# Kernel tuning notes

Measured on AMD Instinct MI355X. Metric: run time of the kernel, lower is better.

Reference implementation:

```python
import jax, jax.numpy as jnp
import numpy as np

N = 50000   # n_nodes (cells)
E = 800000  # n_edges (avg degree 16)
D = 128     # feature dim


def setup_inputs() -> dict:
    key = jax.random.key(0)
    ks = jax.random.split(key, 8)
    x = jax.random.normal(ks[0], (N, D), dtype=jnp.float32)
    src = jax.random.randint(ks[1], (E,), 0, N, dtype=jnp.int32)
    dst = jax.random.randint(ks[2], (E,), 0, N, dtype=jnp.int32)
    vals = jax.random.uniform(ks[3], (E,), dtype=jnp.float32)
    # GraphConvolution weight (dim -> dim), applied as x @ W
    W_gc = jax.random.normal(ks[4], (D, D), dtype=jnp.float32) / np.sqrt(D).astype(np.float32)
    b_gc = jnp.zeros((D,), jnp.float32)
    # linear2: nn.Linear(dim, dim) -> x @ W2.T + b2
    W2 = jax.random.normal(ks[5], (D, D), dtype=jnp.float32) / np.sqrt(D).astype(np.float32)
    b2 = jnp.zeros((D,), jnp.float32)
    return {"x": x, "vals": vals, "W_gc": W_gc, "b_gc": b_gc,
            "W2": W2, "b2": b2, "src": src, "dst": dst}


def reference(x, vals, W_gc, b_gc, W2, b2, src, dst):
    # GraphConvolution (dropout is identity in eval mode):
    #   support = x @ W + b ; out = relu(adj_sparse @ support)
    support = x @ W_gc + b_gc                         # [N, D]
    msg = support[src] * vals[:, None]                # gather rows, scale by edge weight
    agg = jax.ops.segment_sum(msg, dst, num_segments=N)  # SpMM via scatter-add
    x1 = jax.nn.relu(agg)                             # [N, D]
    # linear2 + dropout(eval=identity) + detached L2 row-normalize
    x2 = x1 @ W2.T + b2                               # [N, D]
    nrm = jax.lax.stop_gradient(
        jnp.sqrt(jnp.sum(x2 * x2, axis=1, keepdims=True)))
    return x2 / nrm
```

## Files before the change

kernel.cpp:

```cpp
#include <hip/hip_runtime.h>
#include <hip/hip_bf16.h>

#define N_NODES 50000
#define N_EDGES 800000
#define DIM     128
#define N_STRIPS (N_NODES / 16)
#define N_BKT    196
#define EDGE_CHUNKS 196
#define BCAP     8192
#define EBUF_CAP 7168
#define AGS      68
#define GEMM_BLOCKS ((N_STRIPS + 3) / 4)
#define FRONT_BLOCKS (GEMM_BLOCKS + EDGE_CHUNKS)

typedef short short8 __attribute__((ext_vector_type(8)));
typedef float floatx4 __attribute__((ext_vector_type(4)));

__device__ inline unsigned short f2bf(float f) {
    __hip_bfloat16 h = __float2bfloat16(f);
    return *reinterpret_cast<unsigned short*>(&h);
}

__global__ __launch_bounds__(256) void pre_pack(
    const float* __restrict__ W1, const float* __restrict__ W2,
    uint4* __restrict__ p1, uint4* __restrict__ p2, int* __restrict__ bcnt)
{
    const int blk = blockIdx.x;
    const int t   = threadIdx.x;
    if (blk < 8) {
        const int s    = blk * 256 + t;
        const int lane = s & 63;
        const int nt   = (s >> 6) & 7;
        const int ks   = s >> 9;
        const int m    = lane & 15;
        const int q    = lane >> 4;
        unsigned short e[8];
        #pragma unroll
        for (int j = 0; j < 8; ++j)
            e[j] = f2bf(W1[(ks * 32 + q * 8 + j) * DIM + nt * 16 + m]);
        uint4 o;
        o.x = (unsigned)e[0] | ((unsigned)e[1] << 16);
        o.y = (unsigned)e[2] | ((unsigned)e[3] << 16);
        o.z = (unsigned)e[4] | ((unsigned)e[5] << 16);
        o.w = (unsigned)e[6] | ((unsigned)e[7] << 16);
        p1[s] = o;
    } else if (blk < 16) {
        const int s    = (blk - 8) * 256 + t;
        const int lane = s & 63;
        const int nt   = (s >> 6) & 7;
        const int ks   = s >> 9;
        const int m    = lane & 15;
        const int q    = lane >> 4;
        const float4 f0 = *reinterpret_cast<const float4*>(&W2[(nt * 16 + m) * DIM + ks * 32 + q * 8]);
        const float4 f1 = *reinterpret_cast<const float4*>(&W2[(nt * 16 + m) * DIM + ks * 32 + q * 8 + 4]);
        unsigned short e[8];
        e[0] = f2bf(f0.x); e[1] = f2bf(f0.y); e[2] = f2bf(f0.z); e[3] = f2bf(f0.w);
        e[4] = f2bf(f1.x); e[5] = f2bf(f1.y); e[6] = f2bf(f1.z); e[7] = f2bf(f1.w);
        uint4 o;
        o.x = (unsigned)e[0] | ((unsigned)e[1] << 16);
        o.y = (unsigned)e[2] | ((unsigned)e[3] << 16);
        o.z = (unsigned)e[4] | ((unsigned)e[5] << 16);
        o.w = (unsigned)e[6] | ((unsigned)e[7] << 16);
        p2[s] = o;
    } else {
        bcnt[t] = 0;
    }
}

__global__ __launch_bounds__(256) void front(
    const float* __restrict__ x, const float* __restrict__ bias,
    const int* __restrict__ src, const int* __restrict__ dst,
    const float* __restrict__ vals, const uint4* __restrict__ p1,
    unsigned short* __restrict__ support, int* __restrict__ bcnt,
    int2* __restrict__ bucketed)
{
    __shared__ int bh[256];
    __shared__ int rcur[256];
    const int t = threadIdx.x;

    if (blockIdx.x < GEMM_BLOCKS) {
        const int wave  = t >> 6;
        const int lane  = t & 63;
        const int strip = blockIdx.x * 4 + wave;
        if (strip >= N_STRIPS) return;
        const int m = lane & 15;
        const int q = lane >> 4;
        const int row = strip * 16 + m;

        short8 a[4];
        const float4* xr = reinterpret_cast<const float4*>(&x[(size_t)row * DIM]);
        #pragma unroll
        for (int ks = 0; ks < 4; ++ks) {
            const float4 f0 = xr[ks * 8 + q * 2];
            const float4 f1 = xr[ks * 8 + q * 2 + 1];
            short8 tt;
            tt[0] = (short)f2bf(f0.x); tt[1] = (short)f2bf(f0.y);
            tt[2] = (short)f2bf(f0.z); tt[3] = (short)f2bf(f0.w);
            tt[4] = (short)f2bf(f1.x); tt[5] = (short)f2bf(f1.y);
            tt[6] = (short)f2bf(f1.z); tt[7] = (short)f2bf(f1.w);
            a[ks] = tt;
        }

        floatx4 acc[8];
        #pragma unroll
        for (int nt = 0; nt < 8; ++nt) { acc[nt][0]=0.f; acc[nt][1]=0.f; acc[nt][2]=0.f; acc[nt][3]=0.f; }

        const short8* Bp = (const short8*)p1;
        #pragma unroll
        for (int ks = 0; ks < 4; ++ks) {
            #pragma unroll
            for (int nt = 0; nt < 8; ++nt) {
                const short8 bf = Bp[(ks * 8 + nt) * 64 + lane];
                acc[nt] = __builtin_amdgcn_mfma_f32_16x16x32_bf16(a[ks], bf, acc[nt], 0, 0, 0);
            }
        }

        #pragma unroll
        for (int nt = 0; nt < 8; ++nt) {
            const float bb = bias[nt * 16 + m];
            #pragma unroll
            for (int i = 0; i < 4; ++i) {
                const int r = strip * 16 + q * 4 + i;
                support[(size_t)r * DIM + nt * 16 + m] = f2bf(acc[nt][i] + bb);
            }
        }
    } else {
        const int chunk = blockIdx.x - GEMM_BLOCKS;
        bh[t] = 0;
        __syncthreads();
        const int base   = chunk * 4096;
        const int navail = min(4096, N_EDGES - base);
        const int4* d4 = reinterpret_cast<const int4*>(dst + base);
        #pragma unroll
        for (int i = 0; i < 4; ++i) {
            const int j = t + i * 256;
            if (j * 4 < navail) {
                const int4 d = d4[j];
                atomicAdd(&bh[d.x >> 8], 1);
                atomicAdd(&bh[d.y >> 8], 1);
                atomicAdd(&bh[d.z >> 8], 1);
                atomicAdd(&bh[d.w >> 8], 1);
            }
        }
        __syncthreads();
        rcur[t] = t * BCAP + atomicAdd(&bcnt[t], bh[t]);
        __syncthreads();
        const int4*   s4 = reinterpret_cast<const int4*>(src + base);
        const float4* v4 = reinterpret_cast<const float4*>(vals + base);
        #pragma unroll
        for (int i = 0; i < 4; ++i) {
            const int j = t + i * 256;
            if (j * 4 < navail) {
                const int4   s = s4[j];
                const int4   d = d4[j];
                const float4 v = v4[j];
                int p;
                p = atomicAdd(&rcur[d.x >> 8], 1);
                bucketed[p] = make_int2((s.x & 0xFFFF) | ((d.x & 0xFF) << 16), __float_as_int(v.x));
                p = atomicAdd(&rcur[d.y >> 8], 1);
                bucketed[p] = make_int2((s.y & 0xFFFF) | ((d.y & 0xFF) << 16), __float_as_int(v.y));
                p = atomicAdd(&rcur[d.z >> 8], 1);
                bucketed[p] = make_int2((s.z & 0xFFFF) | ((d.z & 0xFF) << 16), __float_as_int(v.z));
                p = atomicAdd(&rcur[d.w >> 8], 1);
                bucketed[p] = make_int2((s.w & 0xFFFF) | ((d.w & 0xFF) << 16), __float_as_int(v.w));
            }
        }
    }
}

__global__ __launch_bounds__(1024) void agg_gemm2(
    const unsigned int* __restrict__ sup, const int2* __restrict__ bucketed,
    const int* __restrict__ bcnt, const short8* __restrict__ Bp,
    const float* __restrict__ bias, float* __restrict__ out)
{
    __shared__ int2 ebuf[EBUF_CAP];
    __shared__ unsigned int agg[256 * AGS];
    __shared__ int cnt[256];
    __shared__ int coff[256];
    __shared__ int cur[256];

    const int b = blockIdx.x;
    const int t = threadIdx.x;
    int nE = bcnt[b];
    if (nE > EBUF_CAP) nE = EBUF_CAP;
    const int base = b * BCAP;

    if (t < 256) cnt[t] = 0;
    __syncthreads();
    for (int i = t; i < nE; i += 1024)
        atomicAdd(&cnt[(bucketed[base + i].x >> 16) & 255], 1);
    __syncthreads();
    if (t < 256) coff[t] = cnt[t];
    __syncthreads();
    for (int off = 1; off < 256; off <<= 1) {
        int u = 0;
        if (t < 256 && t >= off) u = coff[t - off];
        __syncthreads();
        if (t < 256 && t >= off) coff[t] += u;
        __syncthreads();
    }
    if (t < 256) cur[t] = coff[t] - cnt[t];
    __syncthreads();
    for (int i = t; i < nE; i += 1024) {
        const int2 e = bucketed[base + i];
        const int  n = (e.x >> 16) & 255;
        const int  p = atomicAdd(&cur[n], 1);
        ebuf[p] = e;
    }
    __syncthreads();

    const int w    = t >> 6;
    const int lane = t & 63;
    for (int nl = w * 16; nl < w * 16 + 16; ++nl) {
        const int end = cur[nl];
        const int beg = end - cnt[nl];
        float ax = 0.f, ay = 0.f;
        int j = beg;
        for (; j + 7 < end; j += 8) {
            int2 e[8];
            unsigned int u[8];
            #pragma unroll
            for (int k = 0; k < 8; ++k) e[k] = ebuf[j + k];
            #pragma unroll
            for (int k = 0; k < 8; ++k) u[k] = sup[(size_t)(e[k].x & 0xFFFF) * 64 + lane];
            #pragma unroll
            for (int k = 0; k < 8; ++k) {
                const float v = __int_as_float(e[k].y);
                ax += __uint_as_float(u[k] << 16) * v;
                ay += __uint_as_float(u[k] & 0xffff0000u) * v;
            }
        }
        for (; j + 3 < end; j += 4) {
            int2 e[4];
            unsigned int u[4];
            #pragma unroll
            for (int k = 0; k < 4; ++k) e[k] = ebuf[j + k];
            #pragma unroll
            for (int k = 0; k < 4; ++k) u[k] = sup[(size_t)(e[k].x & 0xFFFF) * 64 + lane];
            #pragma unroll
            for (int k = 0; k < 4; ++k) {
                const float v = __int_as_float(e[k].y);
                ax += __uint_as_float(u[k] << 16) * v;
                ay += __uint_as_float(u[k] & 0xffff0000u) * v;
            }
        }
        for (; j < end; ++j) {
            const int2 e0 = ebuf[j];
            const unsigned int u0 = sup[(size_t)(e0.x & 0xFFFF) * 64 + lane];
            const float v0 = __int_as_float(e0.y);
            ax += __uint_as_float(u0 << 16) * v0;
            ay += __uint_as_float(u0 & 0xffff0000u) * v0;
        }
        ax = fmaxf(ax, 0.f);
        ay = fmaxf(ay, 0.f);
        agg[nl * AGS + lane] = (unsigned int)f2bf(ax) | ((unsigned int)f2bf(ay) << 16);
    }
    __syncthreads();

    const int row0 = b * 256 + w * 16;
    if (row0 >= N_NODES) return;
    const int m = lane & 15;
    const int q = lane >> 4;

    short8 a[4];
    #pragma unroll
    for (int ks = 0; ks < 4; ++ks) {
        const uint4 t4 = *reinterpret_cast<const uint4*>(&agg[(w * 16 + m) * AGS + ks * 16 + q * 4]);
        a[ks] = *reinterpret_cast<const short8*>(&t4);
    }

    floatx4 acc[8];
    #pragma unroll
    for (int nt = 0; nt < 8; ++nt) { acc[nt][0]=0.f; acc[nt][1]=0.f; acc[nt][2]=0.f; acc[nt][3]=0.f; }

    #pragma unroll
    for (int ks = 0; ks < 4; ++ks) {
        #pragma unroll
        for (int nt = 0; nt < 8; ++nt) {
            const short8 bf = Bp[(ks * 8 + nt) * 64 + lane];
            acc[nt] = __builtin_amdgcn_mfma_f32_16x16x32_bf16(a[ks], bf, acc[nt], 0, 0, 0);
        }
    }

    #pragma unroll
    for (int nt = 0; nt < 8; ++nt) {
        const float bb = bias[nt * 16 + m];
        #pragma unroll
        for (int i = 0; i < 4; ++i) acc[nt][i] += bb;
    }

    float sq[4] = {0.f, 0.f, 0.f, 0.f};
    #pragma unroll
    for (int nt = 0; nt < 8; ++nt)
        #pragma unroll
        for (int i = 0; i < 4; ++i) sq[i] += acc[nt][i] * acc[nt][i];
    #pragma unroll
    for (int i = 0; i < 4; ++i) {
        #pragma unroll
        for (int mask = 1; mask < 16; mask <<= 1)
            sq[i] += __shfl_xor(sq[i], mask);
        sq[i] = 1.0f / sqrtf(sq[i]);
    }

    #pragma unroll
    for (int nt = 0; nt < 8; ++nt) {
        #pragma unroll
        for (int i = 0; i < 4; ++i) {
            const int r = row0 + q * 4 + i;
            out[(size_t)r * DIM + nt * 16 + m] = acc[nt][i] * sq[i];
        }
    }
}

extern "C" void kernel_launch(void* const* d_in, const int* in_sizes, int n_in,
                              void* d_out, int out_size, void* d_ws, size_t ws_size,
                              hipStream_t stream) {
    const float* x    = (const float*)d_in[0];
    const float* vals = (const float*)d_in[1];
    const float* W_gc = (const float*)d_in[2];
    const float* b_gc = (const float*)d_in[3];
    const float* W2   = (const float*)d_in[4];
    const float* b2   = (const float*)d_in[5];
    const int*   src  = (const int*)d_in[6];
    const int*   dst  = (const int*)d_in[7];

    float* out = (float*)d_out;

    const size_t SUP_B = (size_t)N_NODES * DIM * 2;
    const size_t BUK_B = (size_t)N_BKT * BCAP * 8;
    char* wsb = (char*)d_ws;
    unsigned short* support = (unsigned short*)wsb;
    int2* bucketed = (int2*)(wsb + SUP_B);
    int*  bcnt     = (int*)(wsb + SUP_B + BUK_B);
    uint4* pw1     = (uint4*)(wsb + SUP_B + BUK_B + 1024);
    uint4* pw2     = (uint4*)(wsb + SUP_B + BUK_B + 1024 + 32768);

    pre_pack<<<17, 256, 0, stream>>>(W_gc, W2, pw1, pw2, bcnt);

    front<<<FRONT_BLOCKS, 256, 0, stream>>>(
        x, b_gc, src, dst, vals, pw1, support, bcnt, bucketed);

    agg_gemm2<<<N_BKT, 1024, 0, stream>>>(
        (const unsigned int*)support, bucketed, bcnt, (const short8*)pw2, b2, out);
}
```

Before: 150.6 us.

## Shrink buckets to 64 nodes, 256-thread agg blocks, 16B-per-lane edge-parallel gathers

Destination buckets shrink from 256 to 64 nodes, giving 782 aggregation blocks of 256 threads instead of 196 blocks of 1024, which spreads work across more CUs. The gather loop now has each quarter-wave handle a different edge and load 16 bytes per lane, followed by a cross-lane shuffle reduction, instead of one 4-byte load per lane per edge. Edge-bucketing blocks are also placed before the GEMM blocks in the front kernel. The smaller per-bucket capacity (1408 edges) raises the risk of overflow and silent truncation on skewed degree distributions.

```diff
diff --git a/kernel.cpp b/kernel.cpp
--- a/kernel.cpp
+++ b/kernel.cpp
@@ -5,10 +5,10 @@
 #define N_EDGES 800000
 #define DIM     128
 #define N_STRIPS (N_NODES / 16)
-#define N_BKT    196
+#define N_BKT    782
 #define EDGE_CHUNKS 196
-#define BCAP     8192
-#define EBUF_CAP 7168
+#define BCAP     1536
+#define EBUF_CAP 1408
 #define AGS      68
 #define GEMM_BLOCKS ((N_STRIPS + 3) / 4)
 #define FRONT_BLOCKS (GEMM_BLOCKS + EDGE_CHUNKS)
@@ -63,7 +63,7 @@
         o.w = (unsigned)e[6] | ((unsigned)e[7] << 16);
         p2[s] = o;
     } else {
-        bcnt[t] = 0;
+        for (int i = t; i < 800; i += 256) bcnt[i] = 0;
     }
 }
 
@@ -74,14 +74,56 @@
     unsigned short* __restrict__ support, int* __restrict__ bcnt,
     int2* __restrict__ bucketed)
 {
-    __shared__ int bh[256];
-    __shared__ int rcur[256];
+    __shared__ int bh[800];
+    __shared__ int rcur[800];
     const int t = threadIdx.x;
 
-    if (blockIdx.x < GEMM_BLOCKS) {
+    if (blockIdx.x < EDGE_CHUNKS) {
+        const int chunk = blockIdx.x;
+        for (int i = t; i < 800; i += 256) bh[i] = 0;
+        __syncthreads();
+        const int base   = chunk * 4096;
+        const int navail = min(4096, N_EDGES - base);
+        const int4* d4 = reinterpret_cast<const int4*>(dst + base);
+        #pragma unroll
+        for (int i = 0; i < 4; ++i) {
+            const int j = t + i * 256;
+            if (j * 4 < navail) {
+                const int4 d = d4[j];
+                atomicAdd(&bh[d.x >> 6], 1);
+                atomicAdd(&bh[d.y >> 6], 1);
+                atomicAdd(&bh[d.z >> 6], 1);
+                atomicAdd(&bh[d.w >> 6], 1);
+            }
+        }
+        __syncthreads();
+        for (int b = t; b < N_BKT; b += 256)
+            rcur[b] = b * BCAP + atomicAdd(&bcnt[b], bh[b]);
+        __syncthreads();
+        const int4*   s4 = reinterpret_cast<const int4*>(src + base);
+        const float4* v4 = reinterpret_cast<const float4*>(vals + base);
+        #pragma unroll
+        for (int i = 0; i < 4; ++i) {
+            const int j = t + i * 256;
+            if (j * 4 < navail) {
+                const int4   s = s4[j];
+                const int4   d = d4[j];
+                const float4 v = v4[j];
+                int p;
+                p = atomicAdd(&rcur[d.x >> 6], 1);
+                bucketed[p] = make_int2((s.x & 0xFFFF) | ((d.x & 63) << 16), __float_as_int(v.x));
+                p = atomicAdd(&rcur[d.y >> 6], 1);
+                bucketed[p] = make_int2((s.y & 0xFFFF) | ((d.y & 63) << 16), __float_as_int(v.y));
+                p = atomicAdd(&rcur[d.z >> 6], 1);
+                bucketed[p] = make_int2((s.z & 0xFFFF) | ((d.z & 63) << 16), __float_as_int(v.z));
+                p = atomicAdd(&rcur[d.w >> 6], 1);
+                bucketed[p] = make_int2((s.w & 0xFFFF) | ((d.w & 63) << 16), __float_as_int(v.w));
+            }
+        }
+    } else {
         const int wave  = t >> 6;
         const int lane  = t & 63;
-        const int strip = blockIdx.x * 4 + wave;
+        const int strip = (blockIdx.x - EDGE_CHUNKS) * 4 + wave;
         if (strip >= N_STRIPS) return;
         const int m = lane & 15;
         const int q = lane >> 4;
@@ -124,60 +166,19 @@
                 support[(size_t)r * DIM + nt * 16 + m] = f2bf(acc[nt][i] + bb);
             }
         }
-    } else {
-        const int chunk = blockIdx.x - GEMM_BLOCKS;
-        bh[t] = 0;
-        __syncthreads();
-        const int base   = chunk * 4096;
-        const int navail = min(4096, N_EDGES - base);
-        const int4* d4 = reinterpret_cast<const int4*>(dst + base);
-        #pragma unroll
-        for (int i = 0; i < 4; ++i) {
-            const int j = t + i * 256;
-            if (j * 4 < navail) {
-                const int4 d = d4[j];
-                atomicAdd(&bh[d.x >> 8], 1);
-                atomicAdd(&bh[d.y >> 8], 1);
-                atomicAdd(&bh[d.z >> 8], 1);
-                atomicAdd(&bh[d.w >> 8], 1);
-            }
-        }
-        __syncthreads();
-        rcur[t] = t * BCAP + atomicAdd(&bcnt[t], bh[t]);
-        __syncthreads();
-        const int4*   s4 = reinterpret_cast<const int4*>(src + base);
-        const float4* v4 = reinterpret_cast<const float4*>(vals + base);
-        #pragma unroll
-        for (int i = 0; i < 4; ++i) {
-            const int j = t + i * 256;
-            if (j * 4 < navail) {
-                const int4   s = s4[j];
-                const int4   d = d4[j];
-                const float4 v = v4[j];
-                int p;
-                p = atomicAdd(&rcur[d.x >> 8], 1);
-                bucketed[p] = make_int2((s.x & 0xFFFF) | ((d.x & 0xFF) << 16), __float_as_int(v.x));
-                p = atomicAdd(&rcur[d.y >> 8], 1);
-                bucketed[p] = make_int2((s.y & 0xFFFF) | ((d.y & 0xFF) << 16), __float_as_int(v.y));
-                p = atomicAdd(&rcur[d.z >> 8], 1);
-                bucketed[p] = make_int2((s.z & 0xFFFF) | ((d.z & 0xFF) << 16), __float_as_int(v.z));
-                p = atomicAdd(&rcur[d.w >> 8], 1);
-                bucketed[p] = make_int2((s.w & 0xFFFF) | ((d.w & 0xFF) << 16), __float_as_int(v.w));
-            }
-        }
-    }
-}
-
-__global__ __launch_bounds__(1024) void agg_gemm2(
+    }
+}
+
+__global__ __launch_bounds__(256) void agg_gemm2(
     const unsigned int* __restrict__ sup, const int2* __restrict__ bucketed,
     const int* __restrict__ bcnt, const short8* __restrict__ Bp,
     const float* __restrict__ bias, float* __restrict__ out)
 {
     __shared__ int2 ebuf[EBUF_CAP];
-    __shared__ unsigned int agg[256 * AGS];
-    __shared__ int cnt[256];
-    __shared__ int coff[256];
-    __shared__ int cur[256];
+    __shared__ unsigned int agg[64 * AGS];
+    __shared__ int cnt[64];
+    __shared__ int coff[64];
+    __shared__ int cur[64];
 
     const int b = blockIdx.x;
     const int t = threadIdx.x;
@@ -185,25 +186,25 @@
     if (nE > EBUF_CAP) nE = EBUF_CAP;
     const int base = b * BCAP;
 
-    if (t < 256) cnt[t] = 0;
-    __syncthreads();
-    for (int i = t; i < nE; i += 1024)
-        atomicAdd(&cnt[(bucketed[base + i].x >> 16) & 255], 1);
-    __syncthreads();
-    if (t < 256) coff[t] = cnt[t];
-    __syncthreads();
-    for (int off = 1; off < 256; off <<= 1) {
+    if (t < 64) cnt[t] = 0;
+    __syncthreads();
+    for (int i = t; i < nE; i += 256)
+        atomicAdd(&cnt[(bucketed[base + i].x >> 16) & 63], 1);
+    __syncthreads();
+    if (t < 64) coff[t] = cnt[t];
+    __syncthreads();
+    for (int off = 1; off < 64; off <<= 1) {
         int u = 0;
-        if (t < 256 && t >= off) u = coff[t - off];
-        __syncthreads();
-        if (t < 256 && t >= off) coff[t] += u;
-        __syncthreads();
-    }
-    if (t < 256) cur[t] = coff[t] - cnt[t];
-    __syncthreads();
-    for (int i = t; i < nE; i += 1024) {
+        if (t < 64 && t >= off) u = coff[t - off];
+        __syncthreads();
+        if (t < 64 && t >= off) coff[t] += u;
+        __syncthreads();
+    }
+    if (t < 64) cur[t] = coff[t] - cnt[t];
+    __syncthreads();
+    for (int i = t; i < nE; i += 256) {
         const int2 e = bucketed[base + i];
-        const int  n = (e.x >> 16) & 255;
+        const int  n = (e.x >> 16) & 63;
         const int  p = atomicAdd(&cur[n], 1);
         ebuf[p] = e;
     }
@@ -211,53 +212,55 @@
 
     const int w    = t >> 6;
     const int lane = t & 63;
+    const int g    = lane >> 4;
+    const int dl   = lane & 15;
+
     for (int nl = w * 16; nl < w * 16 + 16; ++nl) {
         const int end = cur[nl];
-        const int beg = end - cnt[nl];
-        float ax = 0.f, ay = 0.f;
-        int j = beg;
-        for (; j + 7 < end; j += 8) {
-            int2 e[8];
-            unsigned int u[8];
-            #pragma unroll
-            for (int k = 0; k < 8; ++k) e[k] = ebuf[j + k];
-            #pragma unroll
-            for (int k = 0; k < 8; ++k) u[k] = sup[(size_t)(e[k].x & 0xFFFF) * 64 + lane];
-            #pragma unroll
-            for (int k = 0; k < 8; ++k) {
-                const float v = __int_as_float(e[k].y);
-                ax += __uint_as_float(u[k] << 16) * v;
-                ay += __uint_as_float(u[k] & 0xffff0000u) * v;
-            }
-        }
-        for (; j + 3 < end; j += 4) {
-            int2 e[4];
-            unsigned int u[4];
-            #pragma unroll
-            for (int k = 0; k < 4; ++k) e[k] = ebuf[j + k];
-            #pragma unroll
-            for (int k = 0; k < 4; ++k) u[k] = sup[(size_t)(e[k].x & 0xFFFF) * 64 + lane];
-            #pragma unroll
-            for (int k = 0; k < 4; ++k) {
-                const float v = __int_as_float(e[k].y);
-                ax += __uint_as_float(u[k] << 16) * v;
-                ay += __uint_as_float(u[k] & 0xffff0000u) * v;
-            }
-        }
-        for (; j < end; ++j) {
-            const int2 e0 = ebuf[j];
-            const unsigned int u0 = sup[(size_t)(e0.x & 0xFFFF) * 64 + lane];
-            const float v0 = __int_as_float(e0.y);
-            ax += __uint_as_float(u0 << 16) * v0;
-            ay += __uint_as_float(u0 & 0xffff0000u) * v0;
-        }
-        ax = fmaxf(ax, 0.f);
-        ay = fmaxf(ay, 0.f);
-        agg[nl * AGS + lane] = (unsigned int)f2bf(ax) | ((unsigned int)f2bf(ay) << 16);
-    }
-    __syncthreads();
-
-    const int row0 = b * 256 + w * 16;
+        const int c   = cnt[nl];
+        const int beg = end - c;
+        float acc[8];
+        #pragma unroll
+        for (int k = 0; k < 8; ++k) acc[k] = 0.f;
+
+        const int nI = (c + 3) >> 2;
+        auto step = [&](int it) {
+            const int  idx = beg + it * 4 + g;
+            const bool vld = idx < end;
+            const int2 e   = ebuf[vld ? idx : beg];
+            const float val = vld ? __int_as_float(e.y) : 0.f;
+            const uint4 u = *reinterpret_cast<const uint4*>(
+                &sup[(size_t)(e.x & 0xFFFF) * 64 + dl * 4]);
+            acc[0] += __uint_as_float(u.x << 16)          * val;
+            acc[1] += __uint_as_float(u.x & 0xffff0000u)  * val;
+            acc[2] += __uint_as_float(u.y << 16)          * val;
+            acc[3] += __uint_as_float(u.y & 0xffff0000u)  * val;
+            acc[4] += __uint_as_float(u.z << 16)          * val;
+            acc[5] += __uint_as_float(u.z & 0xffff0000u)  * val;
+            acc[6] += __uint_as_float(u.w << 16)          * val;
+            acc[7] += __uint_as_float(u.w & 0xffff0000u)  * val;
+        };
+        int it = 0;
+        for (; it + 3 < nI; it += 4) { step(it); step(it+1); step(it+2); step(it+3); }
+        for (; it < nI; ++it) step(it);
+
+        #pragma unroll
+        for (int k = 0; k < 8; ++k) {
+            acc[k] += __shfl_xor(acc[k], 16);
+            acc[k] += __shfl_xor(acc[k], 32);
+        }
+        if (dl == lane) {
+            uint4 o;
+            o.x = (unsigned)f2bf(fmaxf(acc[0],0.f)) | ((unsigned)f2bf(fmaxf(acc[1],0.f)) << 16);
+            o.y = (unsigned)f2bf(fmaxf(acc[2],0.f)) | ((unsigned)f2bf(fmaxf(acc[3],0.f)) << 16);
+            o.z = (unsigned)f2bf(fmaxf(acc[4],0.f)) | ((unsigned)f2bf(fmaxf(acc[5],0.f)) << 16);
+            o.w = (unsigned)f2bf(fmaxf(acc[6],0.f)) | ((unsigned)f2bf(fmaxf(acc[7],0.f)) << 16);
+            *reinterpret_cast<uint4*>(&agg[nl * AGS + dl * 4]) = o;
+        }
+    }
+    __syncthreads();
+
+    const int row0 = b * 64 + w * 16;
     if (row0 >= N_NODES) return;
     const int m = lane & 15;
     const int q = lane >> 4;
@@ -332,14 +335,14 @@
     unsigned short* support = (unsigned short*)wsb;
     int2* bucketed = (int2*)(wsb + SUP_B);
     int*  bcnt     = (int*)(wsb + SUP_B + BUK_B);
-    uint4* pw1     = (uint4*)(wsb + SUP_B + BUK_B + 1024);
-    uint4* pw2     = (uint4*)(wsb + SUP_B + BUK_B + 1024 + 32768);
+    uint4* pw1     = (uint4*)(wsb + SUP_B + BUK_B + 4096);
+    uint4* pw2     = (uint4*)(wsb + SUP_B + BUK_B + 4096 + 32768);
 
     pre_pack<<<17, 256, 0, stream>>>(W_gc, W2, pw1, pw2, bcnt);
 
     front<<<FRONT_BLOCKS, 256, 0, stream>>>(
         x, b_gc, src, dst, vals, pw1, support, bcnt, bucketed);
 
-    agg_gemm2<<<N_BKT, 1024, 0, stream>>>(
+    agg_gemm2<<<N_BKT, 256, 0, stream>>>(
         (const unsigned int*)support, bucketed, bcnt, (const short8*)pw2, b2, out);
 }
```

Result: no change. 148.4 us (-1.5%).
